# Kernel tuning notes

Hardware: AMD Instinct MI355X
Metric: run time of the kernel (lower is better)

The kernel has to match this reference:

```python
import jax, jax.numpy as jnp
import numpy as np

B, N, C_IN, C_OUT, K = 8, 4096, 64, 128, 15
RADIUS = 0.1            # 2.5 * grid_size(0.04) * sigma(1.0)
MAX_NN = 34
KP_EXTENT = 0.04        # point_influence = prev_grid_size * sigma
KERNEL_RADIUS = 1.5 * KP_EXTENT
NEG_SLOPE = 0.2
BN_EPS = 1e-5


def setup_inputs() -> dict:
    key = jax.random.key(0)
    k1, k2, k3, k4 = jax.random.split(key, 4)
    xyz = jax.random.uniform(k1, (B, N, 3), dtype=jnp.float32)
    feats = jax.random.normal(k2, (B, N, C_IN), dtype=jnp.float32)
    # fixed kernel point disposition inside the kernel ball (requires_grad=False in torch)
    kp = jax.random.normal(k3, (K, 3), dtype=jnp.float32)
    kp = kp / (jnp.linalg.norm(kp, axis=-1, keepdims=True) + 1e-6) * KERNEL_RADIUS * 0.7
    kp = kp.at[0].set(0.0)  # center point
    std = float(np.sqrt(2.0 / (K * C_IN)))
    weight = jax.random.normal(k4, (K, C_IN, C_OUT), dtype=jnp.float32) * std
    gamma = jnp.ones((C_OUT,), dtype=jnp.float32)
    beta = jnp.zeros((C_OUT,), dtype=jnp.float32)
    return {"xyz": xyz, "feats": feats, "K_points": kp, "weight": weight,
            "gamma": gamma, "beta": beta}


def _ball_query(xyz):
    # xyz: [B, N, 3] -> flat neighbor idx [B*N, MAX_NN] into the concatenated
    # point array; missing neighbors get shadow index B*N.
    b_, n_, _ = xyz.shape
    shadow = b_ * n_

    def per_cloud(pts, b):
        d2 = jnp.sum((pts[:, None, :] - pts[None, :, :]) ** 2, axis=-1)  # [N, N]
        neg_d2, idx = jax.lax.top_k(-d2, MAX_NN)                         # k nearest
        valid = (-neg_d2) <= RADIUS ** 2
        return jnp.where(valid, idx + b * n_, shadow)

    return jax.vmap(per_cloud)(xyz, jnp.arange(b_)).reshape(b_ * n_, MAX_NN)


def _kpconv_block(xyz, feats, K_points, weight, gamma, beta):
    b_, n_, _ = xyz.shape
    pts = xyz.reshape(b_ * n_, 3)
    f = feats.reshape(b_ * n_, C_IN)
    nidx = _ball_query(xyz)                                   # [M, nn]
    # shadow point far away / zero features (KPConv_ops)
    pts_pad = jnp.concatenate([pts, jnp.full((1, 3), 1e6, pts.dtype)], axis=0)
    f_pad = jnp.concatenate([f, jnp.zeros((1, C_IN), f.dtype)], axis=0)
    nbr = pts_pad[nidx] - pts[:, None, :]                     # [M, nn, 3] relative coords
    sq = jnp.sum((nbr[:, :, None, :] - K_points) ** 2, -1)    # [M, nn, K]
    w = jnp.maximum(1.0 - jnp.sqrt(sq) / KP_EXTENT, 0.0)      # linear influence
    nf = f_pad[nidx]                                          # [M, nn, Cin]
    wf = jnp.einsum('mnk,mnc->mkc', w, nf)                    # per-kernel-point feats
    out = jnp.einsum('mkc,kcd->md', wf, weight)               # [M, Cout]
    # FastBatchNorm1d (training-mode batch stats, biased var) + LeakyReLU
    mu = out.mean(axis=0)
    var = out.var(axis=0)
    out = (out - mu) * jax.lax.rsqrt(var + BN_EPS) * gamma + beta
    out = jnp.where(out >= 0, out, NEG_SLOPE * out)
    return out.reshape(b_, n_, C_OUT)


def reference(xyz, feats, K_points, weight, gamma, beta):
    return _kpconv_block(xyz, feats, K_points, weight, gamma, beta)
```

## Files before the change

### kernel.cpp

```cpp
#include <hip/hip_runtime.h>


#define NB     8
#define NPTS   4096
#define M_TOT  32768
#define CIN    64
#define COUT   128
#define NKP    15
#define NCELL  1728
#define UCAP   512
#define R2EFF  (0.082f * 0.082f)
#define KP_INV 25.0f
#define NEG_SLOPE 0.2f
#define KCP    1024
#define WFPAD  1032
#define SP     40

typedef float f32x4_t __attribute__((ext_vector_type(4)));
typedef short bf16x8_t __attribute__((ext_vector_type(8)));

__device__ __forceinline__ unsigned short f2bf(float f) {
  union { float f; unsigned u; } v; v.f = f;
  unsigned r = v.u + 0x7FFF + ((v.u >> 16) & 1);
  return (unsigned short)(r >> 16);
}
__device__ __forceinline__ int cell_of(float x, float y, float z) {
  int cx = (int)(x * 12.f); cx = cx > 11 ? 11 : cx;
  int cy = (int)(y * 12.f); cy = cy > 11 ? 11 : cy;
  int cz = (int)(z * 12.f); cz = cz > 11 ? 11 : cz;
  return (cz * 12 + cy) * 12 + cx;
}

__global__ __launch_bounds__(256) void k0a_hist(
    const float* __restrict__ xyz, int* __restrict__ cellcnt)
{
  const int pt = blockIdx.x * 256 + threadIdx.x;
  const float x = xyz[pt * 3], y = xyz[pt * 3 + 1], z = xyz[pt * 3 + 2];
  const int b = pt >> 12;
  atomicAdd(&cellcnt[b * NCELL + cell_of(x, y, z)], 1);
}

__global__ __launch_bounds__(256) void k0b_scan_kW(
    const int* __restrict__ cellcnt, int* __restrict__ cellstart,
    const float* __restrict__ W, unsigned short* __restrict__ Wt)
{
  if (blockIdx.x >= 8) {
    const int idx = (blockIdx.x - 8) * 256 + threadIdx.x;
    const int d = idx & 127, c = idx >> 7;
    union { unsigned short s[16]; uint4 v[2]; } u;
    #pragma unroll
    for (int k = 0; k < NKP; k++)
      u.s[k] = f2bf(W[(size_t)k * (CIN * COUT) + c * COUT + d]);
    u.s[15] = 0;
    uint4* dst = (uint4*)&Wt[(size_t)d * KCP + c * 16];
    dst[0] = u.v[0]; dst[1] = u.v[1];
    return;
  }
  __shared__ int ps[256];
  const int b = blockIdx.x, t = threadIdx.x;
  int local[7], s = 0;
  #pragma unroll
  for (int i = 0; i < 7; i++) {
    const int cid = t * 7 + i;
    const int c = (cid < NCELL) ? cellcnt[b * NCELL + cid] : 0;
    local[i] = c; s += c;
  }
  ps[t] = s; __syncthreads();
  for (int off = 1; off < 256; off <<= 1) {
    int v = (t >= off) ? ps[t - off] : 0;
    __syncthreads();
    ps[t] += v;
    __syncthreads();
  }
  int run = ps[t] - s;
  #pragma unroll
  for (int i = 0; i < 7; i++) {
    const int cid = t * 7 + i;
    if (cid < NCELL) { cellstart[b * 1729 + cid] = run; run += local[i]; }
  }
  if (t == 255) cellstart[b * 1729 + NCELL] = ps[255];
}

__global__ __launch_bounds__(256) void k0c_scatter(
    const float* __restrict__ xyz, const float* __restrict__ feats,
    const int* __restrict__ cellstart, int* __restrict__ cellfill,
    int* __restrict__ qorder, float4* __restrict__ xyzs,
    unsigned short* __restrict__ fsorted)
{
  const int pt = blockIdx.x * 256 + threadIdx.x;
  const float x = xyz[pt * 3], y = xyz[pt * 3 + 1], z = xyz[pt * 3 + 2];
  const int b = pt >> 12;
  const int cid = cell_of(x, y, z);
  const int slot = atomicAdd(&cellfill[b * NCELL + cid], 1);
  const int pos = b * NPTS + cellstart[b * 1729 + cid] + slot;
  qorder[pos] = pt;
  xyzs[pos] = make_float4(x, y, z, 0.f);
  const float* src = &feats[(size_t)pt * CIN];
  uint4* dst = (uint4*)&fsorted[(size_t)pos * CIN];
  #pragma unroll
  for (int g = 0; g < 8; g++) {
    float4 a = *(const float4*)(src + g * 8);
    float4 c = *(const float4*)(src + g * 8 + 4);
    union { unsigned short s[8]; uint4 v; } u;
    u.s[0] = f2bf(a.x); u.s[1] = f2bf(a.y); u.s[2] = f2bf(a.z); u.s[3] = f2bf(a.w);
    u.s[4] = f2bf(c.x); u.s[5] = f2bf(c.y); u.s[6] = f2bf(c.z); u.s[7] = f2bf(c.w);
    dst[g] = u.v;
  }
}

__global__ __launch_bounds__(256, 4) void k2_conv(
    const float4* __restrict__ xyzs, const unsigned short* __restrict__ fsorted,
    const float* __restrict__ kpts, const int* __restrict__ cellstart,
    const int* __restrict__ qorder, const unsigned short* __restrict__ Wt,
    float* __restrict__ out, float* __restrict__ psum,
    float* __restrict__ psumsq)
{
  __shared__ char smraw[33792] __attribute__((aligned(16)));
  float4*         Pu   = (float4*)smraw;
  unsigned short* cpos = (unsigned short*)(smraw + 8192);
  short (*S)[SP]       = (short(*)[SP])(smraw + 8192);
  short (*FT)[SP]      = (short(*)[SP])(smraw + 28672);
  short (*wf)[WFPAD]   = (short(*)[WFPAD])smraw;

  __shared__ float4 qd[16];
  __shared__ int    qm[16];
  __shared__ float  kp[NKP][4];
  __shared__ int    Tsh;
  __shared__ int    ucnt;

  const int tid = threadIdx.x;
  const int w   = tid >> 6;
  const int L   = tid & 63;
  const int m0  = blockIdx.x * 16;
  const int b   = m0 >> 12;

  if (tid >= 64 && tid < 64 + NKP * 3) {
    const int t2 = tid - 64;
    kp[t2 / 3][t2 - (t2 / 3) * 3] = kpts[t2];
  }

  if (tid < 64) {
    int cxm = 12, cym = 12, czm = 12, cxM = -1, cyM = -1, czM = -1;
    if (tid < 16) {
      const float4 Q = xyzs[m0 + tid];
      qd[tid] = Q;
      qm[tid] = qorder[m0 + tid];
      int a = (int)(Q.x * 12.f); a = a > 11 ? 11 : a;
      int c = (int)(Q.y * 12.f); c = c > 11 ? 11 : c;
      int d = (int)(Q.z * 12.f); d = d > 11 ? 11 : d;
      cxm = cxM = a; cym = cyM = c; czm = czM = d;
    }
    #pragma unroll
    for (int off = 8; off >= 1; off >>= 1) {
      int v;
      v = __shfl_xor(cxm, off); cxm = v < cxm ? v : cxm;
      v = __shfl_xor(cxM, off); cxM = v > cxM ? v : cxM;
      v = __shfl_xor(cym, off); cym = v < cym ? v : cym;
      v = __shfl_xor(cyM, off); cyM = v > cyM ? v : cyM;
      v = __shfl_xor(czm, off); czm = v < czm ? v : czm;
      v = __shfl_xor(czM, off); czM = v > czM ? v : czM;
    }
    cxm = __shfl(cxm, 0); cxM = __shfl(cxM, 0);
    cym = __shfl(cym, 0); cyM = __shfl(cyM, 0);
    czm = __shfl(czm, 0); czM = __shfl(czM, 0);

    const int x0 = cxm > 0 ? cxm - 1 : 0, x1 = cxM < 11 ? cxM + 1 : 11;
    const int y0 = cym > 0 ? cym - 1 : 0, y1 = cyM < 11 ? cyM + 1 : 11;
    const int z0 = czm > 0 ? czm - 1 : 0, z1 = czM < 11 ? czM + 1 : 11;
    const int yspan = y1 - y0 + 1;
    int nr = yspan * (z1 - z0 + 1);
    nr = nr > 64 ? 64 : nr;

    int rs = 0, len = 0;
    if (tid < nr) {
      const int zz = z0 + tid / yspan, yy = y0 + tid % yspan;
      const int base = b * 1729 + (zz * 12 + yy) * 12;
      rs  = cellstart[base + x0];
      len = cellstart[base + x1 + 1] - rs;
    }
    int incl = len;
    #pragma unroll
    for (int off = 1; off < 64; off <<= 1) {
      const int v = __shfl_up(incl, off);
      if (tid >= off) incl += v;
    }
    const int excl = incl - len;
    for (int i = 0; i < len; i++) cpos[excl + i] = (unsigned short)(rs + i);
    if (tid == 63) Tsh = incl;
    if (tid == 62) ucnt = 0;
  }
  __syncthreads();
  const int T = Tsh;

  for (int tb = 0; tb < T; tb += 256) {
    const int t = tb + tid;
    if (t < T) {
      const int pos = (int)cpos[t];
      const float4 P = xyzs[b * NPTS + pos];
      float best = 1e9f;
      #pragma unroll
      for (int i = 0; i < 16; i++) {
        const float4 Q = qd[i];
        const float dx = P.x - Q.x, dy = P.y - Q.y, dz = P.z - Q.z;
        const float d2 = dx * dx + dy * dy + dz * dz;
        best = d2 < best ? d2 : best;
      }
      if (best <= R2EFF) {
        const int slot = atomicAdd(&ucnt, 1);
        if (slot < UCAP)
          Pu[slot] = make_float4(P.x, P.y, P.z, __int_as_float(pos));
      }
    }
  }
  __syncthreads();
  int U = ucnt; U = U > UCAP ? UCAP : U;

  const int ln = L & 15;
  const int kh = L >> 4;

  f32x4_t acc[16];
  #pragma unroll
  for (int mt = 0; mt < 16; mt++) acc[mt] = (f32x4_t){0.f, 0.f, 0.f, 0.f};

  for (int ub = 0; ub < U; ub += 32) {
    {
      const int c  = tid & 63;
      const int i0 = tid >> 6;
      #pragma unroll
      for (int ii = 0; ii < 8; ii++) {
        const int i = ii * 4 + i0;
        const int u = ub + i;
        short v = 0;
        if (u < U) {
          const int pos = __float_as_int(Pu[u].w);
          v = (short)fsorted[(size_t)(b * NPTS + pos) * CIN + c];
        }
        FT[c][i] = v;
      }
    }
    #pragma unroll
    for (int rep = 0; rep < 2; rep++) {
      const int p = rep * 256 + tid;
      const int q = p >> 5;
      const int n = p & 31;
      const int u = ub + n;
      if (u < U) {
        const float4 P = Pu[u];
        const float4 Q = qd[q];
        const float rx = P.x - Q.x, ry = P.y - Q.y, rz = P.z - Q.z;
        #pragma unroll
        for (int k = 0; k < NKP; k++) {
          const float dx = rx - kp[k][0];
          const float dy = ry - kp[k][1];
          const float dz = rz - kp[k][2];
          const float wv =
              fmaxf(1.f - sqrtf(dx * dx + dy * dy + dz * dz) * KP_INV, 0.f);
          S[q * 16 + k][n] = (short)f2bf(wv);
        }
        S[q * 16 + 15][n] = 0;
      } else {
        #pragma unroll
        for (int k = 0; k < 16; k++) S[q * 16 + k][n] = 0;
      }
    }
    __syncthreads();

    bf16x8_t bb = *(const bf16x8_t*)&FT[w * 16 + ln][kh * 8];
    #pragma unroll
    for (int mt = 0; mt < 16; mt++) {
      bf16x8_t aa = *(const bf16x8_t*)&S[mt * 16 + ln][kh * 8];
      acc[mt] = __builtin_amdgcn_mfma_f32_16x16x32_bf16(aa, bb, acc[mt],
                                                        0, 0, 0);
    }
    __syncthreads();
  }

  #pragma unroll
  for (int mt = 0; mt < 16; mt++) {
    union { unsigned short s[4]; unsigned long long d; } u;
    #pragma unroll
    for (int j = 0; j < 4; j++) u.s[j] = f2bf(acc[mt][j]);
    *(unsigned long long*)&wf[mt][(w * 16 + ln) * 16 + kh * 4] = u.d;
  }
  __syncthreads();

  const int colbase = w * 32;

  f32x4_t acc2[2];
  acc2[0] = (f32x4_t){0.f, 0.f, 0.f, 0.f};
  acc2[1] = (f32x4_t){0.f, 0.f, 0.f, 0.f};

  const unsigned short* Bp0 = &Wt[(size_t)(colbase + ln) * KCP + kh * 8];
  const unsigned short* Bp1 = Bp0 + 16 * KCP;
  const short* Ap = &wf[ln][kh * 8];

  #pragma unroll 4
  for (int kk = 0; kk < 32; kk++) {
    const int ko = kk * 32;
    bf16x8_t b0 = *(const bf16x8_t*)(Bp0 + ko);
    bf16x8_t b1 = *(const bf16x8_t*)(Bp1 + ko);
    bf16x8_t a0 = *(const bf16x8_t*)(Ap + ko);
    acc2[0] = __builtin_amdgcn_mfma_f32_16x16x32_bf16(a0, b0, acc2[0], 0, 0, 0);
    acc2[1] = __builtin_amdgcn_mfma_f32_16x16x32_bf16(a0, b1, acc2[1], 0, 0, 0);
  }

  float s0 = 0.f, q0 = 0.f, s1 = 0.f, q1 = 0.f;
  #pragma unroll
  for (int j = 0; j < 4; j++) {
    s0 += acc2[0][j]; q0 += acc2[0][j] * acc2[0][j];
    s1 += acc2[1][j]; q1 += acc2[1][j] * acc2[1][j];
  }
  s0 += __shfl_xor(s0, 16); s0 += __shfl_xor(s0, 32);
  q0 += __shfl_xor(q0, 16); q0 += __shfl_xor(q0, 32);
  s1 += __shfl_xor(s1, 16); s1 += __shfl_xor(s1, 32);
  q1 += __shfl_xor(q1, 16); q1 += __shfl_xor(q1, 32);
  if (kh == 0) {
    atomicAdd(&psum[colbase + ln], s0);
    atomicAdd(&psumsq[colbase + ln], q0);
    atomicAdd(&psum[colbase + 16 + ln], s1);
    atomicAdd(&psumsq[colbase + 16 + ln], q1);
  }

  #pragma unroll
  for (int c = 0; c < 2; c++) {
    #pragma unroll
    for (int j = 0; j < 4; j++) {
      const int row = kh * 4 + j;
      out[(size_t)qm[row] * COUT + colbase + c * 16 + ln] = acc2[c][j];
    }
  }
}

__global__ __launch_bounds__(256) void k4_norm(
    float* __restrict__ out, const float* __restrict__ psum,
    const float* __restrict__ psumsq, const float* __restrict__ gamma,
    const float* __restrict__ beta)
{
  __shared__ float a_s[128], b_s[128];
  if (threadIdx.x < 128) {
    const int d = threadIdx.x;
    double mu  = (double)psum[d] / (double)M_TOT;
    double var = (double)psumsq[d] / (double)M_TOT - mu * mu;
    float rstd = (float)(1.0 / sqrt(var + 1e-5));
    float a = rstd * gamma[d];
    a_s[d] = a;
    b_s[d] = beta[d] - (float)mu * a;
  }
  __syncthreads();
  const int idx = blockIdx.x * 256 + threadIdx.x;
  float4 v = ((const float4*)out)[idx];
  const int d0 = (idx * 4) & 127;
  float y0 = v.x * a_s[d0 + 0] + b_s[d0 + 0];
  float y1 = v.y * a_s[d0 + 1] + b_s[d0 + 1];
  float y2 = v.z * a_s[d0 + 2] + b_s[d0 + 2];
  float y3 = v.w * a_s[d0 + 3] + b_s[d0 + 3];
  v.x = y0 >= 0.f ? y0 : NEG_SLOPE * y0;
  v.y = y1 >= 0.f ? y1 : NEG_SLOPE * y1;
  v.z = y2 >= 0.f ? y2 : NEG_SLOPE * y2;
  v.w = y3 >= 0.f ? y3 : NEG_SLOPE * y3;
  ((float4*)out)[idx] = v;
}

extern "C" void kernel_launch(void* const* d_in, const int* in_sizes, int n_in,
                              void* d_out, int out_size, void* d_ws,
                              size_t ws_size, hipStream_t stream)
{
  const float* xyz   = (const float*)d_in[0];
  const float* feats = (const float*)d_in[1];
  const float* kpts  = (const float*)d_in[2];
  const float* W     = (const float*)d_in[3];
  const float* gamma = (const float*)d_in[4];
  const float* beta  = (const float*)d_in[5];
  float* out = (float*)d_out;

  char* ws = (char*)d_ws;
  int*            cellcnt   = (int*)(ws + 0);
  int*            cellfill  = (int*)(ws + 55296);
  float*          psum      = (float*)(ws + 110592);
  float*          psumsq    = (float*)(ws + 111104);
  int*            cellstart = (int*)(ws + 111616);
  int*            qorder    = (int*)(ws + 167040);
  float4*         xyzs      = (float4*)(ws + 298112);
  unsigned short* fsorted   = (unsigned short*)(ws + 822400);
  unsigned short* Wt        = (unsigned short*)(ws + 5016704);

  hipMemsetAsync(ws, 0, 111616, stream);

  k0a_hist   <<< 128, 256, 0, stream>>>(xyz, cellcnt);
  k0b_scan_kW<<<  40, 256, 0, stream>>>(cellcnt, cellstart, W, Wt);
  k0c_scatter<<< 128, 256, 0, stream>>>(xyz, feats, cellstart, cellfill,
                                        qorder, xyzs, fsorted);
  k2_conv    <<<2048, 256, 0, stream>>>(xyzs, fsorted, kpts, cellstart,
                                        qorder, Wt, out, psum, psumsq);
  k4_norm    <<<(out_size / 4) / 256, 256, 0, stream>>>(out, psum, psumsq,
                                                        gamma, beta);
}
```

Measured before the change: 196.7 us.

## Fuse preprocessing and conv+batchnorm into cooperative kernels with grid syncs

Replaces the memset, histogram, scan/weight-transpose and scatter launches with one cooperative kernel that separates its phases with grid-wide syncs. The conv kernel becomes a cooperative kernel in which each block processes two tiles and keeps their results in registers. After a grid sync it applies batchnorm and LeakyReLU directly, so the separate normalization pass that re-read and re-wrote the output is gone. This removes several launch gaps and one full round trip of the output through memory. The cost is grid-sync overhead, the loss of the spare blocks that could hide imbalance, and a dependency on cooperative-launch support, with a fallback to the old path.

```diff
diff --git a/kernel.cpp b/kernel.cpp
--- a/kernel.cpp
+++ b/kernel.cpp
@@ -1,4 +1,7 @@
 #include <hip/hip_runtime.h>
+#include <hip/hip_cooperative_groups.h>
+
+namespace cg = cooperative_groups;
 
 
 #define NB     8
@@ -31,6 +34,87 @@
   return (cz * 12 + cy) * 12 + cx;
 }
 
+__global__ __launch_bounds__(256) void kpre_coop(
+    const float* __restrict__ xyz, const float* __restrict__ feats,
+    const float* __restrict__ W,
+    int* __restrict__ cellcnt,
+    int* __restrict__ cellfill, int* __restrict__ cellstart,
+    int* __restrict__ qorder, float4* __restrict__ xyzs,
+    unsigned short* __restrict__ fsorted, unsigned short* __restrict__ Wt)
+{
+  cg::grid_group grid = cg::this_grid();
+  __shared__ int ps[256];
+  const int tid = threadIdx.x;
+  const int idx = blockIdx.x * 256 + tid;
+
+  if (idx < 27904) cellcnt[idx] = 0;
+  grid.sync();
+
+  {
+    const float x = xyz[idx * 3], y = xyz[idx * 3 + 1], z = xyz[idx * 3 + 2];
+    const int b = idx >> 12;
+    atomicAdd(&cellcnt[b * NCELL + cell_of(x, y, z)], 1);
+  }
+  grid.sync();
+
+  if (blockIdx.x >= 8 && blockIdx.x < 40) {
+    const int i2 = (blockIdx.x - 8) * 256 + tid;
+    const int d = i2 & 127, c = i2 >> 7;
+    union { unsigned short s[16]; uint4 v[2]; } u;
+    #pragma unroll
+    for (int k = 0; k < NKP; k++)
+      u.s[k] = f2bf(W[(size_t)k * (CIN * COUT) + c * COUT + d]);
+    u.s[15] = 0;
+    uint4* dst = (uint4*)&Wt[(size_t)d * KCP + c * 16];
+    dst[0] = u.v[0]; dst[1] = u.v[1];
+  } else if (blockIdx.x < 8) {
+    const int b = blockIdx.x, t = tid;
+    int local[7], s = 0;
+    #pragma unroll
+    for (int i = 0; i < 7; i++) {
+      const int cid = t * 7 + i;
+      const int c = (cid < NCELL) ? cellcnt[b * NCELL + cid] : 0;
+      local[i] = c; s += c;
+    }
+    ps[t] = s; __syncthreads();
+    for (int off = 1; off < 256; off <<= 1) {
+      int v = (t >= off) ? ps[t - off] : 0;
+      __syncthreads();
+      ps[t] += v;
+      __syncthreads();
+    }
+    int run = ps[t] - s;
+    #pragma unroll
+    for (int i = 0; i < 7; i++) {
+      const int cid = t * 7 + i;
+      if (cid < NCELL) { cellstart[b * 1729 + cid] = run; run += local[i]; }
+    }
+    if (t == 255) cellstart[b * 1729 + NCELL] = ps[255];
+  }
+  grid.sync();
+
+  {
+    const float x = xyz[idx * 3], y = xyz[idx * 3 + 1], z = xyz[idx * 3 + 2];
+    const int b = idx >> 12;
+    const int cid = cell_of(x, y, z);
+    const int slot = atomicAdd(&cellfill[b * NCELL + cid], 1);
+    const int pos = b * NPTS + cellstart[b * 1729 + cid] + slot;
+    qorder[pos] = idx;
+    xyzs[pos] = make_float4(x, y, z, 0.f);
+    const float* src = &feats[(size_t)idx * CIN];
+    uint4* dst = (uint4*)&fsorted[(size_t)pos * CIN];
+    #pragma unroll
+    for (int g = 0; g < 8; g++) {
+      float4 a = *(const float4*)(src + g * 8);
+      float4 c = *(const float4*)(src + g * 8 + 4);
+      union { unsigned short s[8]; uint4 v; } u;
+      u.s[0] = f2bf(a.x); u.s[1] = f2bf(a.y); u.s[2] = f2bf(a.z); u.s[3] = f2bf(a.w);
+      u.s[4] = f2bf(c.x); u.s[5] = f2bf(c.y); u.s[6] = f2bf(c.z); u.s[7] = f2bf(c.w);
+      dst[g] = u.v;
+    }
+  }
+}
+
 __global__ __launch_bounds__(256) void k0a_hist(
     const float* __restrict__ xyz, int* __restrict__ cellcnt)
 {
@@ -108,36 +192,29 @@
   }
 }
 
-__global__ __launch_bounds__(256, 4) void k2_conv(
+__device__ __forceinline__ void conv_tile(
+    const int bt,
     const float4* __restrict__ xyzs, const unsigned short* __restrict__ fsorted,
-    const float* __restrict__ kpts, const int* __restrict__ cellstart,
-    const int* __restrict__ qorder, const unsigned short* __restrict__ Wt,
-    float* __restrict__ out, float* __restrict__ psum,
-    float* __restrict__ psumsq)
-{
-  __shared__ char smraw[33792] __attribute__((aligned(16)));
+    const int* __restrict__ cellstart, const int* __restrict__ qorder,
+    const unsigned short* __restrict__ Wt,
+    float* __restrict__ psum, float* __restrict__ psumsq,
+    char* smraw, float4* qd, int* qm, float (*kp)[4],
+    int* Tsh_p, int* ucnt_p,
+    f32x4_t acc2[2], int rows[4])
+{
   float4*         Pu   = (float4*)smraw;
   unsigned short* cpos = (unsigned short*)(smraw + 8192);
   short (*S)[SP]       = (short(*)[SP])(smraw + 8192);
   short (*FT)[SP]      = (short(*)[SP])(smraw + 28672);
   short (*wf)[WFPAD]   = (short(*)[WFPAD])smraw;
 
-  __shared__ float4 qd[16];
-  __shared__ int    qm[16];
-  __shared__ float  kp[NKP][4];
-  __shared__ int    Tsh;
-  __shared__ int    ucnt;
-
   const int tid = threadIdx.x;
   const int w   = tid >> 6;
   const int L   = tid & 63;
-  const int m0  = blockIdx.x * 16;
+  const int m0  = bt * 16;
   const int b   = m0 >> 12;
 
-  if (tid >= 64 && tid < 64 + NKP * 3) {
-    const int t2 = tid - 64;
-    kp[t2 / 3][t2 - (t2 / 3) * 3] = kpts[t2];
-  }
+  __syncthreads();
 
   if (tid < 64) {
     int cxm = 12, cym = 12, czm = 12, cxM = -1, cyM = -1, czM = -1;
@@ -186,11 +263,11 @@
     }
     const int excl = incl - len;
     for (int i = 0; i < len; i++) cpos[excl + i] = (unsigned short)(rs + i);
-    if (tid == 63) Tsh = incl;
-    if (tid == 62) ucnt = 0;
+    if (tid == 63) *Tsh_p = incl;
+    if (tid == 62) *ucnt_p = 0;
   }
   __syncthreads();
-  const int T = Tsh;
+  const int T = *Tsh_p;
 
   for (int tb = 0; tb < T; tb += 256) {
     const int t = tb + tid;
@@ -206,14 +283,14 @@
         best = d2 < best ? d2 : best;
       }
       if (best <= R2EFF) {
-        const int slot = atomicAdd(&ucnt, 1);
+        const int slot = atomicAdd(ucnt_p, 1);
         if (slot < UCAP)
           Pu[slot] = make_float4(P.x, P.y, P.z, __int_as_float(pos));
       }
     }
   }
   __syncthreads();
-  int U = ucnt; U = U > UCAP ? UCAP : U;
+  int U = *ucnt_p; U = U > UCAP ? UCAP : U;
 
   const int ln = L & 15;
   const int kh = L >> 4;
@@ -286,7 +363,6 @@
 
   const int colbase = w * 32;
 
-  f32x4_t acc2[2];
   acc2[0] = (f32x4_t){0.f, 0.f, 0.f, 0.f};
   acc2[1] = (f32x4_t){0.f, 0.f, 0.f, 0.f};
 
@@ -322,12 +398,109 @@
   }
 
   #pragma unroll
+  for (int j = 0; j < 4; j++) rows[j] = qm[kh * 4 + j];
+}
+
+__global__ __launch_bounds__(256, 4) void k2_coop(
+    const float4* __restrict__ xyzs, const unsigned short* __restrict__ fsorted,
+    const float* __restrict__ kpts, const int* __restrict__ cellstart,
+    const int* __restrict__ qorder, const unsigned short* __restrict__ Wt,
+    float* __restrict__ out, float* __restrict__ psum,
+    float* __restrict__ psumsq, const float* __restrict__ gamma,
+    const float* __restrict__ beta)
+{
+  __shared__ char smraw[33792] __attribute__((aligned(16)));
+  __shared__ float4 qd[16];
+  __shared__ int    qm[16];
+  __shared__ float  kp[NKP][4];
+  __shared__ int    Tsh;
+  __shared__ int    ucnt;
+
+  const int tid = threadIdx.x;
+  if (tid >= 64 && tid < 64 + NKP * 3) {
+    const int t2 = tid - 64;
+    kp[t2 / 3][t2 - (t2 / 3) * 3] = kpts[t2];
+  }
+
+  f32x4_t aA[2], aB[2];
+  int rA[4], rB[4];
+  conv_tile(blockIdx.x, xyzs, fsorted, cellstart, qorder, Wt, psum, psumsq,
+            smraw, qd, qm, kp, &Tsh, &ucnt, aA, rA);
+  conv_tile(blockIdx.x + 1024, xyzs, fsorted, cellstart, qorder, Wt, psum,
+            psumsq, smraw, qd, qm, kp, &Tsh, &ucnt, aB, rB);
+
+  cg::this_grid().sync();
+
+  float* a_s = (float*)smraw;
+  float* b_s = (float*)(smraw + 512);
+  if (tid < 128) {
+    const float s  = __hip_atomic_load(&psum[tid], __ATOMIC_RELAXED,
+                                       __HIP_MEMORY_SCOPE_AGENT);
+    const float sq = __hip_atomic_load(&psumsq[tid], __ATOMIC_RELAXED,
+                                       __HIP_MEMORY_SCOPE_AGENT);
+    double mu  = (double)s / (double)M_TOT;
+    double var = (double)sq / (double)M_TOT - mu * mu;
+    float rstd = (float)(1.0 / sqrt(var + 1e-5));
+    float a = rstd * gamma[tid];
+    a_s[tid] = a;
+    b_s[tid] = beta[tid] - (float)mu * a;
+  }
+  __syncthreads();
+
+  const int w  = tid >> 6;
+  const int L  = tid & 63;
+  const int ln = L & 15;
+  const int colbase = w * 32;
+  #pragma unroll
   for (int c = 0; c < 2; c++) {
+    const int col = colbase + c * 16 + ln;
+    const float a = a_s[col], bb = b_s[col];
     #pragma unroll
     for (int j = 0; j < 4; j++) {
-      const int row = kh * 4 + j;
-      out[(size_t)qm[row] * COUT + colbase + c * 16 + ln] = acc2[c][j];
-    }
+      float yA = aA[c][j] * a + bb;
+      yA = yA >= 0.f ? yA : NEG_SLOPE * yA;
+      out[(size_t)rA[j] * COUT + col] = yA;
+      float yB = aB[c][j] * a + bb;
+      yB = yB >= 0.f ? yB : NEG_SLOPE * yB;
+      out[(size_t)rB[j] * COUT + col] = yB;
+    }
+  }
+}
+
+__global__ __launch_bounds__(256, 4) void k2_plain(
+    const float4* __restrict__ xyzs, const unsigned short* __restrict__ fsorted,
+    const float* __restrict__ kpts, const int* __restrict__ cellstart,
+    const int* __restrict__ qorder, const unsigned short* __restrict__ Wt,
+    float* __restrict__ out, float* __restrict__ psum,
+    float* __restrict__ psumsq)
+{
+  __shared__ char smraw[33792] __attribute__((aligned(16)));
+  __shared__ float4 qd[16];
+  __shared__ int    qm[16];
+  __shared__ float  kp[NKP][4];
+  __shared__ int    Tsh;
+  __shared__ int    ucnt;
+
+  const int tid = threadIdx.x;
+  if (tid >= 64 && tid < 64 + NKP * 3) {
+    const int t2 = tid - 64;
+    kp[t2 / 3][t2 - (t2 / 3) * 3] = kpts[t2];
+  }
+
+  f32x4_t acc2[2];
+  int rows[4];
+  conv_tile(blockIdx.x, xyzs, fsorted, cellstart, qorder, Wt, psum, psumsq,
+            smraw, qd, qm, kp, &Tsh, &ucnt, acc2, rows);
+
+  const int w  = tid >> 6;
+  const int L  = tid & 63;
+  const int ln = L & 15;
+  const int colbase = w * 32;
+  #pragma unroll
+  for (int c = 0; c < 2; c++) {
+    #pragma unroll
+    for (int j = 0; j < 4; j++)
+      out[(size_t)rows[j] * COUT + colbase + c * 16 + ln] = acc2[c][j];
   }
 }
 
@@ -384,13 +557,51 @@
   unsigned short* fsorted   = (unsigned short*)(ws + 822400);
   unsigned short* Wt        = (unsigned short*)(ws + 5016704);
 
+  static int coop_mode = -1;
+  if (coop_mode < 0) {
+    int dev = 0;
+    (void)hipGetDevice(&dev);
+    int coop = 0;
+    (void)hipDeviceGetAttribute(&coop, hipDeviceAttributeCooperativeLaunch, dev);
+    hipDeviceProp_t prop;
+    int ncu = 0;
+    if (hipGetDeviceProperties(&prop, dev) == hipSuccess)
+      ncu = prop.multiProcessorCount;
+    int occ2 = 0, occp = 0;
+    (void)hipOccupancyMaxActiveBlocksPerMultiprocessor(
+        &occ2, (const void*)k2_coop, 256, 0);
+    (void)hipOccupancyMaxActiveBlocksPerMultiprocessor(
+        &occp, (const void*)kpre_coop, 256, 0);
+    coop_mode = (coop && ncu > 0 && occ2 * ncu >= 1024 && occp * ncu >= 128)
+                    ? 1 : 0;
+  }
+
+  if (coop_mode == 1) {
+    void* pre_args[] = {(void*)&xyz, (void*)&feats, (void*)&W,
+                        (void*)&cellcnt, (void*)&cellfill, (void*)&cellstart,
+                        (void*)&qorder, (void*)&xyzs, (void*)&fsorted,
+                        (void*)&Wt};
+    hipError_t e1 = hipLaunchCooperativeKernel(
+        (const void*)kpre_coop, dim3(128), dim3(256), pre_args, 0, stream);
+    if (e1 == hipSuccess) {
+      void* k2_args[] = {(void*)&xyzs, (void*)&fsorted, (void*)&kpts,
+                         (void*)&cellstart, (void*)&qorder, (void*)&Wt,
+                         (void*)&out, (void*)&psum, (void*)&psumsq,
+                         (void*)&gamma, (void*)&beta};
+      hipError_t e2 = hipLaunchCooperativeKernel(
+          (const void*)k2_coop, dim3(1024), dim3(256), k2_args, 0, stream);
+      if (e2 == hipSuccess) return;
+    }
+    (void)hipGetLastError();
+    coop_mode = 0;
+  }
+
   hipMemsetAsync(ws, 0, 111616, stream);
-
   k0a_hist   <<< 128, 256, 0, stream>>>(xyz, cellcnt);
   k0b_scan_kW<<<  40, 256, 0, stream>>>(cellcnt, cellstart, W, Wt);
   k0c_scatter<<< 128, 256, 0, stream>>>(xyz, feats, cellstart, cellfill,
                                         qorder, xyzs, fsorted);
-  k2_conv    <<<2048, 256, 0, stream>>>(xyzs, fsorted, kpts, cellstart,
+  k2_plain   <<<2048, 256, 0, stream>>>(xyzs, fsorted, kpts, cellstart,
                                         qorder, Wt, out, psum, psumsq);
   k4_norm    <<<(out_size / 4) / 256, 256, 0, stream>>>(out, psum, psumsq,
                                                         gamma, beta);
```

Result: no change. 197.2 us (+0.3%).

## Drop padded kernel-point slot, swizzle wf layout, split S stage into halves

Applied to the files above, without the earlier changes.

Changes the reduction layout from 16 padded kernel-point slots per channel to 15×64 k-major rows (KCP 960), cutting the second GEMM from 32 to 30 MFMA steps and storing wf with an XOR swizzle to avoid LDS bank conflicts. The S tile is now computed in two halves of 8 query rows interleaved with MFMAs, shrinking shared memory (UCAP 512→400) so occupancy can rise to 5 blocks per SM. Kernel-point distance uses the expanded |r|²−2r·k+|k|² form with a raw sqrt intrinsic and a faster, non-ties-to-even bf16 rounding. Costs are an extra barrier per tile, slightly different numerics, and possible truncation if more than 400 neighbour candidates appear.

```diff
diff --git a/kernel.cpp b/kernel.cpp
--- a/kernel.cpp
+++ b/kernel.cpp
@@ -8,12 +8,12 @@
 #define COUT   128
 #define NKP    15
 #define NCELL  1728
-#define UCAP   512
+#define UCAP   400
 #define R2EFF  (0.082f * 0.082f)
 #define KP_INV 25.0f
 #define NEG_SLOPE 0.2f
-#define KCP    1024
-#define WFPAD  1032
+#define KCP    960
+#define WFROW  1920
 #define SP     40
 
 typedef float f32x4_t __attribute__((ext_vector_type(4)));
@@ -23,6 +23,10 @@
   union { float f; unsigned u; } v; v.f = f;
   unsigned r = v.u + 0x7FFF + ((v.u >> 16) & 1);
   return (unsigned short)(r >> 16);
+}
+__device__ __forceinline__ unsigned short f2bf_fast(float f) {
+  union { float f; unsigned u; } v; v.f = f;
+  return (unsigned short)((v.u + 0x8000u) >> 16);
 }
 __device__ __forceinline__ int cell_of(float x, float y, float z) {
   int cx = (int)(x * 12.f); cx = cx > 11 ? 11 : cx;
@@ -46,14 +50,11 @@
 {
   if (blockIdx.x >= 8) {
     const int idx = (blockIdx.x - 8) * 256 + threadIdx.x;
-    const int d = idx & 127, c = idx >> 7;
-    union { unsigned short s[16]; uint4 v[2]; } u;
+    const int c = idx & 63, d = idx >> 6;
     #pragma unroll
     for (int k = 0; k < NKP; k++)
-      u.s[k] = f2bf(W[(size_t)k * (CIN * COUT) + c * COUT + d]);
-    u.s[15] = 0;
-    uint4* dst = (uint4*)&Wt[(size_t)d * KCP + c * 16];
-    dst[0] = u.v[0]; dst[1] = u.v[1];
+      Wt[(size_t)d * KCP + k * 64 + c] =
+          f2bf(W[(size_t)k * (CIN * COUT) + c * COUT + d]);
     return;
   }
   __shared__ int ps[256];
@@ -108,19 +109,18 @@
   }
 }
 
-__global__ __launch_bounds__(256, 4) void k2_conv(
+__global__ __launch_bounds__(256, 5) void k2_conv(
     const float4* __restrict__ xyzs, const unsigned short* __restrict__ fsorted,
     const float* __restrict__ kpts, const int* __restrict__ cellstart,
     const int* __restrict__ qorder, const unsigned short* __restrict__ Wt,
     float* __restrict__ out, float* __restrict__ psum,
     float* __restrict__ psumsq)
 {
-  __shared__ char smraw[33792] __attribute__((aligned(16)));
+  __shared__ char smraw[32000] __attribute__((aligned(16)));
   float4*         Pu   = (float4*)smraw;
-  unsigned short* cpos = (unsigned short*)(smraw + 8192);
-  short (*S)[SP]       = (short(*)[SP])(smraw + 8192);
-  short (*FT)[SP]      = (short(*)[SP])(smraw + 28672);
-  short (*wf)[WFPAD]   = (short(*)[WFPAD])smraw;
+  unsigned short* cpos = (unsigned short*)(smraw + 6400);
+  short (*S)[SP]       = (short(*)[SP])(smraw + 6400);
+  short (*FT)[SP]      = (short(*)[SP])(smraw + 26880);
 
   __shared__ float4 qd[16];
   __shared__ int    qm[16];
@@ -134,9 +134,11 @@
   const int m0  = blockIdx.x * 16;
   const int b   = m0 >> 12;
 
-  if (tid >= 64 && tid < 64 + NKP * 3) {
-    const int t2 = tid - 64;
-    kp[t2 / 3][t2 - (t2 / 3) * 3] = kpts[t2];
+  if (tid >= 64 && tid < 64 + NKP) {
+    const int k = tid - 64;
+    const float kx = kpts[k * 3], ky = kpts[k * 3 + 1], kz = kpts[k * 3 + 2];
+    kp[k][0] = -2.f * kx; kp[k][1] = -2.f * ky; kp[k][2] = -2.f * kz;
+    kp[k][3] = kx * kx + ky * ky + kz * kz;
   }
 
   if (tid < 64) {
@@ -217,6 +219,8 @@
 
   const int ln = L & 15;
   const int kh = L >> 4;
+  const int qh = tid >> 5;
+  const int nn = tid & 31;
 
   f32x4_t acc[16];
   #pragma unroll
@@ -238,49 +242,60 @@
         FT[c][i] = v;
       }
     }
-    #pragma unroll
-    for (int rep = 0; rep < 2; rep++) {
-      const int p = rep * 256 + tid;
-      const int q = p >> 5;
-      const int n = p & 31;
-      const int u = ub + n;
-      if (u < U) {
-        const float4 P = Pu[u];
-        const float4 Q = qd[q];
-        const float rx = P.x - Q.x, ry = P.y - Q.y, rz = P.z - Q.z;
-        #pragma unroll
-        for (int k = 0; k < NKP; k++) {
-          const float dx = rx - kp[k][0];
-          const float dy = ry - kp[k][1];
-          const float dz = rz - kp[k][2];
-          const float wv =
-              fmaxf(1.f - sqrtf(dx * dx + dy * dy + dz * dz) * KP_INV, 0.f);
-          S[q * 16 + k][n] = (short)f2bf(wv);
+
+    bf16x8_t bb;
+    #pragma unroll
+    for (int half = 0; half < 2; half++) {
+      {
+        const int u = ub + nn;
+        if (u < U) {
+          const float4 P = Pu[u];
+          const float4 Q = qd[half * 8 + qh];
+          const float rx = P.x - Q.x, ry = P.y - Q.y, rz = P.z - Q.z;
+          const float rr = rx * rx + ry * ry + rz * rz;
+          #pragma unroll
+          for (int k = 0; k < NKP; k++) {
+            float d2 = fmaf(kp[k][0], rx,
+                       fmaf(kp[k][1], ry,
+                       fmaf(kp[k][2], rz, rr + kp[k][3])));
+            d2 = fmaxf(d2, 0.f);
+            const float wv =
+                fmaxf(fmaf(-KP_INV, __builtin_amdgcn_sqrtf(d2), 1.f), 0.f);
+            S[qh * 16 + k][nn] = (short)f2bf_fast(wv);
+          }
+          S[qh * 16 + 15][nn] = 0;
+        } else {
+          #pragma unroll
+          for (int k = 0; k < 16; k++) S[qh * 16 + k][nn] = 0;
         }
-        S[q * 16 + 15][n] = 0;
-      } else {
-        #pragma unroll
-        for (int k = 0; k < 16; k++) S[q * 16 + k][n] = 0;
-      }
-    }
-    __syncthreads();
-
-    bf16x8_t bb = *(const bf16x8_t*)&FT[w * 16 + ln][kh * 8];
+      }
+      __syncthreads();
+      if (half == 0) bb = *(const bf16x8_t*)&FT[w * 16 + ln][kh * 8];
+      #pragma unroll
+      for (int mt = 0; mt < 8; mt++) {
+        bf16x8_t aa = *(const bf16x8_t*)&S[mt * 16 + ln][kh * 8];
+        acc[half * 8 + mt] =
+            __builtin_amdgcn_mfma_f32_16x16x32_bf16(aa, bb, acc[half * 8 + mt],
+                                                    0, 0, 0);
+      }
+      __syncthreads();
+    }
+  }
+
+  {
+    const int c = w * 16 + ln;
     #pragma unroll
     for (int mt = 0; mt < 16; mt++) {
-      bf16x8_t aa = *(const bf16x8_t*)&S[mt * 16 + ln][kh * 8];
-      acc[mt] = __builtin_amdgcn_mfma_f32_16x16x32_bf16(aa, bb, acc[mt],
-                                                        0, 0, 0);
-    }
-    __syncthreads();
-  }
-
-  #pragma unroll
-  for (int mt = 0; mt < 16; mt++) {
-    union { unsigned short s[4]; unsigned long long d; } u;
-    #pragma unroll
-    for (int j = 0; j < 4; j++) u.s[j] = f2bf(acc[mt][j]);
-    *(unsigned long long*)&wf[mt][(w * 16 + ln) * 16 + kh * 4] = u.d;
+      #pragma unroll
+      for (int j = 0; j < 4; j++) {
+        const int k = kh * 4 + j;
+        if (k < 15) {
+          int byteo = mt * WFROW + ((k * 64 + c) << 1);
+          byteo ^= (mt & 7) << 4;
+          *(unsigned short*)(smraw + byteo) = f2bf_fast(acc[mt][j]);
+        }
+      }
+    }
   }
   __syncthreads();
 
@@ -292,14 +307,16 @@
 
   const unsigned short* Bp0 = &Wt[(size_t)(colbase + ln) * KCP + kh * 8];
   const unsigned short* Bp1 = Bp0 + 16 * KCP;
-  const short* Ap = &wf[ln][kh * 8];
-
-  #pragma unroll 4
-  for (int kk = 0; kk < 32; kk++) {
-    const int ko = kk * 32;
+  const char* wfb = (const char*)smraw + ln * WFROW;
+  const int   sw  = (ln & 7) << 4;
+
+  #pragma unroll 6
+  for (int kk = 0; kk < 30; kk++) {
+    const int ko  = kk * 32;
+    const int inr = (kh * 16 + kk * 64) ^ sw;
     bf16x8_t b0 = *(const bf16x8_t*)(Bp0 + ko);
     bf16x8_t b1 = *(const bf16x8_t*)(Bp1 + ko);
-    bf16x8_t a0 = *(const bf16x8_t*)(Ap + ko);
+    bf16x8_t a0 = *(const bf16x8_t*)(wfb + inr);
     acc2[0] = __builtin_amdgcn_mfma_f32_16x16x32_bf16(a0, b0, acc2[0], 0, 0, 0);
     acc2[1] = __builtin_amdgcn_mfma_f32_16x16x32_bf16(a0, b1, acc2[1], 0, 0, 0);
   }
```

New measurement: 195.9 us. Within noise of the previous version (-0.4%).
